# Optimization experiments

Measured on AMD Instinct MI355X. Metric: run time of the kernel, lower is better.

Reference implementation:

```python
import jax, jax.numpy as jnp
import numpy as np

NUM_GRAPHS = 16  # static number of graphs for pooling
BN_EPS = 1e-5


def gat_layer(x, W, a_src, a_dst, src, dst, N, concat):
    # x: (N, Fin), W: (H, Fin, Fout), a_src/a_dst: (H, Fout)
    Wh = jnp.einsum('ni,hio->hno', x, W)                      # (H, N, Fout)
    e_src = jnp.einsum('hno,ho->hn', Wh, a_src)               # (H, N)
    e_dst = jnp.einsum('hno,ho->hn', Wh, a_dst)               # (H, N)
    e = jax.nn.leaky_relu(e_src[:, src] + e_dst[:, dst], 0.2)  # (H, E)
    # edge softmax over incoming edges per dst; torch code starts max at 0
    seg_max = jax.vmap(lambda eh: jax.ops.segment_max(eh, dst, num_segments=N))(e)
    e_max = jnp.maximum(seg_max, 0.0)                         # (H, N)
    exp_e = jnp.exp(e - e_max[:, dst])                        # (H, E)
    exp_sum = jax.vmap(lambda eh: jax.ops.segment_sum(eh, dst, num_segments=N))(exp_e)
    attn = exp_e / (exp_sum[:, dst] + 1e-8)                   # (H, E)
    msgs = attn[:, :, None] * Wh[:, src]                      # (H, E, Fout)
    out = jax.vmap(lambda m: jax.ops.segment_sum(m, dst, num_segments=N))(msgs)  # (H, N, Fout)
    if concat:
        out = jnp.transpose(out, (1, 0, 2)).reshape(N, -1)
    else:
        out = out.mean(axis=0)
    return out, attn


def batchnorm(h, gamma, beta):
    mu = h.mean(axis=0)
    var = h.var(axis=0)
    return (h - mu) / jnp.sqrt(var + BN_EPS) * gamma + beta


def setup_inputs() -> dict:
    key = jax.random.key(0)
    ks = jax.random.split(key, 20)
    N, E = 50000, 400000
    IN, HID, H, NC = 262, 128, 4, 2

    def xavier(k, shape):
        fan_in, fan_out = shape[-2], shape[-1]
        lim = np.sqrt(6.0 / (fan_in + fan_out))
        return jax.random.uniform(k, shape, jnp.float32, -lim, lim)

    x = jax.random.normal(ks[0], (N, IN), jnp.float32)
    edge_index = jax.random.randint(ks[1], (2, E), 0, N, jnp.int64)
    batch = jnp.sort(jax.random.randint(ks[2], (N,), 0, NUM_GRAPHS, jnp.int64))

    return {
        'x': x, 'edge_index': edge_index, 'batch': batch,
        'W1': xavier(ks[3], (H, IN, HID)),
        'a_src1': xavier(ks[4], (H, HID, 1)).squeeze(-1),
        'a_dst1': xavier(ks[5], (H, HID, 1)).squeeze(-1),
        'W2': xavier(ks[6], (1, HID * H, HID)),
        'a_src2': xavier(ks[7], (1, HID, 1)).squeeze(-1),
        'a_dst2': xavier(ks[8], (1, HID, 1)).squeeze(-1),
        'bn1_g': jnp.ones((HID * H,), jnp.float32),
        'bn1_b': jnp.zeros((HID * H,), jnp.float32),
        'bn2_g': jnp.ones((HID,), jnp.float32),
        'bn2_b': jnp.zeros((HID,), jnp.float32),
        'cls_w1': xavier(ks[9], (HID, HID // 2)),
        'cls_b1': jnp.zeros((HID // 2,), jnp.float32),
        'cls_w2': xavier(ks[10], (HID // 2, NC)),
        'cls_b2': jnp.zeros((NC,), jnp.float32),
        'ep_w1': xavier(ks[11], (HID * 2, HID)),
        'ep_b1': jnp.zeros((HID,), jnp.float32),
        'ep_w2': xavier(ks[12], (HID, 1)),
        'ep_b2': jnp.zeros((1,), jnp.float32),
    }


def reference(x, edge_index, batch, W1, a_src1, a_dst1, W2, a_src2, a_dst2,
              bn1_g, bn1_b, bn2_g, bn2_b, cls_w1, cls_b1, cls_w2, cls_b2,
              ep_w1, ep_b1, ep_w2, ep_b2):
    N = x.shape[0]
    src, dst = edge_index[0], edge_index[1]

    h1, _ = gat_layer(x, W1, a_src1, a_dst1, src, dst, N, concat=True)
    h1 = batchnorm(jax.nn.elu(h1), bn1_g, bn1_b)

    h2, attn2 = gat_layer(h1, W2, a_src2, a_dst2, src, dst, N, concat=False)
    h2 = batchnorm(jax.nn.elu(h2), bn2_g, bn2_b)

    # global mean pool over graphs
    sums = jax.ops.segment_sum(h2, batch, num_segments=NUM_GRAPHS)
    counts = jax.ops.segment_sum(jnp.ones((N,), h2.dtype), batch, num_segments=NUM_GRAPHS)
    graph_repr = sums / jnp.clip(counts, 1.0)[:, None]

    logits = jax.nn.relu(graph_repr @ cls_w1 + cls_b1) @ cls_w2 + cls_b2

    edge_feat = jnp.concatenate([h2[src], h2[dst]], axis=1)  # (E, 2*hidden)
    importance = jax.nn.sigmoid(
        (jax.nn.relu(edge_feat @ ep_w1 + ep_b1) @ ep_w2 + ep_b2).squeeze(-1))

    gat_attention = jnp.transpose(attn2, (1, 0))  # (E, 1)
    return logits, h2, importance, gat_attention
```

## Files before the change

### kernel.cpp

```cpp
#include <hip/hip_runtime.h>
#include <hip/hip_bf16.h>
#include <math.h>

typedef __hip_bfloat16 bf16;
typedef __bf16 bf16x8 __attribute__((ext_vector_type(8)));
typedef __bf16 bf16x2v __attribute__((ext_vector_type(2)));
typedef float f32x4 __attribute__((ext_vector_type(4)));

#define NN 50000
#define EE 400000
#define FIN 262
#define KP1 288
#define HID 128
#define NH 4
#define C1 512
#define NGR 16
#define SCAN_NB ((NN + 255) / 256)

__device__ __forceinline__ float b2f(bf16 x){ return __bfloat162float(x); }
__device__ __forceinline__ bf16 f2b(float x){ return __float2bfloat16(x); }
__device__ __forceinline__ float lrelu(float v){ return v >= 0.f ? v : 0.2f * v; }
__device__ __forceinline__ float eluf(float v){ return v > 0.f ? v : expm1f(v); }

__global__ void zero_words(unsigned int* __restrict__ p, int n) {
  int i = blockIdx.x * 256 + threadIdx.x;
  if (i < n) p[i] = 0u;
}

__global__ __launch_bounds__(256)
void gemm_mfma(const bf16* __restrict__ A, const bf16* __restrict__ Bt,
               bf16* __restrict__ C, int M, int K, int Ncols,
               const float* __restrict__ sc, const float* __restrict__ sh) {
  __shared__ __align__(16) __bf16 As[128 * 40];
  __shared__ __align__(16) __bf16 Bs[128 * 40];
  int bm = blockIdx.y * 128, bn = blockIdx.x * 128;
  int tid = threadIdx.x;
  int wave = tid >> 6, lane = tid & 63;
  int quad = lane >> 4, l16 = lane & 15;
  int wm = (wave >> 1) * 64, wn = (wave & 1) * 64;
  f32x4 acc[4][4];
  #pragma unroll
  for (int i = 0; i < 4; ++i)
    #pragma unroll
    for (int j = 0; j < 4; ++j)
      acc[i][j] = (f32x4){0.f, 0.f, 0.f, 0.f};

  for (int k0 = 0; k0 < K; k0 += 32) {
    #pragma unroll
    for (int l = 0; l < 2; ++l) {
      int e = l * 2048 + tid * 8;
      int row = e >> 5, col = e & 31;
      uint4 va = {0u, 0u, 0u, 0u};
      int gm = bm + row;
      if (gm < M) {
        va = *(const uint4*)(A + (size_t)gm * K + k0 + col);
        if (sc) {
          bf16x8 a8 = *(bf16x8*)&va;
          float4 c0 = *(const float4*)(sc + k0 + col);
          float4 c1 = *(const float4*)(sc + k0 + col + 4);
          float4 h0 = *(const float4*)(sh + k0 + col);
          float4 h1v = *(const float4*)(sh + k0 + col + 4);
          bf16x8 t8;
          t8[0] = (__bf16)((float)a8[0] * c0.x + h0.x);
          t8[1] = (__bf16)((float)a8[1] * c0.y + h0.y);
          t8[2] = (__bf16)((float)a8[2] * c0.z + h0.z);
          t8[3] = (__bf16)((float)a8[3] * c0.w + h0.w);
          t8[4] = (__bf16)((float)a8[4] * c1.x + h1v.x);
          t8[5] = (__bf16)((float)a8[5] * c1.y + h1v.y);
          t8[6] = (__bf16)((float)a8[6] * c1.z + h1v.z);
          t8[7] = (__bf16)((float)a8[7] * c1.w + h1v.w);
          va = *(uint4*)&t8;
        }
      }
      *(uint4*)(&As[row * 40 + col]) = va;
      uint4 vb = {0u, 0u, 0u, 0u};
      int gn = bn + row;
      if (gn < Ncols) vb = *(const uint4*)(Bt + (size_t)gn * K + k0 + col);
      *(uint4*)(&Bs[row * 40 + col]) = vb;
    }
    __syncthreads();
    bf16x8 af[4], bf_[4];
    #pragma unroll
    for (int i = 0; i < 4; ++i)
      af[i] = *(const bf16x8*)(&As[(wm + i * 16 + l16) * 40 + quad * 8]);
    #pragma unroll
    for (int j = 0; j < 4; ++j)
      bf_[j] = *(const bf16x8*)(&Bs[(wn + j * 16 + l16) * 40 + quad * 8]);
    #pragma unroll
    for (int i = 0; i < 4; ++i)
      #pragma unroll
      for (int j = 0; j < 4; ++j)
        acc[i][j] = __builtin_amdgcn_mfma_f32_16x16x32_bf16(af[i], bf_[j], acc[i][j], 0, 0, 0);
    __syncthreads();
  }
  #pragma unroll
  for (int i = 0; i < 4; ++i) {
    #pragma unroll
    for (int r = 0; r < 4; ++r) {
      int gm = bm + wm + i * 16 + quad * 4 + r;
      if (gm >= M) continue;
      #pragma unroll
      for (int j = 0; j < 4; ++j) {
        int gn = bn + wn + j * 16 + l16;
        C[(size_t)gm * Ncols + gn] = f2b(acc[i][j][r]);
      }
    }
  }
}

__global__ void conv_x(const float* __restrict__ x, bf16* __restrict__ xb) {
  int i = blockIdx.x * 256 + threadIdx.x;
  if (i >= NN * KP1) return;
  int row = i / KP1, col = i - row * KP1;
  xb[i] = (col < FIN) ? f2b(x[(size_t)row * FIN + col]) : f2b(0.f);
}
__global__ void prep_b1t(const float* __restrict__ W1, bf16* __restrict__ B1t) {
  int i = blockIdx.x * 256 + threadIdx.x;
  if (i >= C1 * KP1) return;
  int n = i / KP1, k = i - n * KP1;
  int h = n >> 7, o = n & 127;
  B1t[i] = (k < FIN) ? f2b(W1[((size_t)h * FIN + k) * HID + o]) : f2b(0.f);
}
__global__ void prep_b2t(const float* __restrict__ W2, bf16* __restrict__ B2t) {
  int i = blockIdx.x * 256 + threadIdx.x;
  if (i >= HID * C1) return;
  int n = i >> 9, k = i & 511;
  B2t[i] = f2b(W2[(size_t)k * HID + n]);
}
__global__ void prep_bpt(const float* __restrict__ epw1, bf16* __restrict__ BPt) {
  int i = blockIdx.x * 256 + threadIdx.x;
  if (i >= 256 * HID) return;
  int n = i >> 7, k = i & 127;
  float v = (n < 128) ? epw1[(size_t)k * HID + n] : epw1[(size_t)(128 + k) * HID + (n - 128)];
  BPt[i] = f2b(v);
}

__global__ void edot_all(const bf16* __restrict__ Wh1, const float* __restrict__ av,
                         const float* __restrict__ bv, float* __restrict__ es1,
                         float* __restrict__ ed1) {
  int wid = threadIdx.x >> 6, lane = threadIdx.x & 63;
  int n = blockIdx.x * 4 + wid;
  if (n >= NN) return;
  int h = lane >> 4, c16 = lane & 15;
  int fbase = h * HID + c16 * 8;
  bf16x8 r = *(const bf16x8*)(Wh1 + (size_t)n * C1 + fbase);
  float s1 = 0.f, s2 = 0.f;
  #pragma unroll
  for (int j = 0; j < 8; ++j) {
    float rv = (float)r[j];
    s1 += rv * av[fbase + j];
    s2 += rv * bv[fbase + j];
  }
  #pragma unroll
  for (int off = 8; off > 0; off >>= 1) {
    s1 += __shfl_xor(s1, off);
    s2 += __shfl_xor(s2, off);
  }
  if (c16 == 0) { es1[n * 4 + h] = s1; ed1[n * 4 + h] = s2; }
}

__global__ void edot1(const bf16* __restrict__ Wh, const float* __restrict__ av,
                      const float* __restrict__ bv, float* __restrict__ es,
                      float* __restrict__ ed) {
  int wid = threadIdx.x >> 6, lane = threadIdx.x & 63;
  int r = blockIdx.x * 4 + wid;
  if (r >= NN) return;
  const bf16* row = Wh + (size_t)r * HID;
  float w0 = b2f(row[lane]), w1 = b2f(row[lane + 64]);
  float s1 = w0 * av[lane] + w1 * av[lane + 64];
  float s2 = w0 * bv[lane] + w1 * bv[lane + 64];
  #pragma unroll
  for (int off = 32; off > 0; off >>= 1) {
    s1 += __shfl_xor(s1, off);
    s2 += __shfl_xor(s2, off);
  }
  if (lane == 0) { es[r] = s1; ed[r] = s2; }
}

__global__ void count_kernel(const int* __restrict__ dst, int* __restrict__ deg, int E) {
  int e = blockIdx.x * blockDim.x + threadIdx.x;
  if (e >= E) return;
  int d = dst[e];
  if ((unsigned)d < NN) atomicAdd(&deg[d], 1);
}

__global__ void scan_p1(const int* __restrict__ deg, int* __restrict__ bsum) {
  __shared__ int s[256];
  int t = threadIdx.x;
  int i = blockIdx.x * 256 + t;
  s[t] = (i < NN) ? deg[i] : 0;
  __syncthreads();
  #pragma unroll
  for (int off = 128; off > 0; off >>= 1) {
    if (t < off) s[t] += s[t + off];
    __syncthreads();
  }
  if (t == 0) bsum[blockIdx.x] = s[0];
}
__global__ void scan_p2(const int* __restrict__ bsum, int* __restrict__ boff,
                        int* __restrict__ total_out) {
  __shared__ int s[256];
  int t = threadIdx.x;
  s[t] = (t < SCAN_NB) ? bsum[t] : 0;
  __syncthreads();
  if (t == 0) {
    int r = 0;
    for (int i = 0; i < SCAN_NB; ++i) { int v = s[i]; s[i] = r; r += v; }
    total_out[0] = r;
  }
  __syncthreads();
  if (t < SCAN_NB) boff[t] = s[t];
}
__global__ void scan_p3(const int* __restrict__ deg, const int* __restrict__ boff,
                        int* __restrict__ rowptr, int* __restrict__ cursor) {
  __shared__ int s[256];
  int t = threadIdx.x;
  int i = blockIdx.x * 256 + t;
  int v = (i < NN) ? deg[i] : 0;
  s[t] = v;
  __syncthreads();
  #pragma unroll
  for (int off = 1; off < 256; off <<= 1) {
    int add = (t >= off) ? s[t - off] : 0;
    __syncthreads();
    s[t] += add;
    __syncthreads();
  }
  if (i < NN) {
    int pos = boff[blockIdx.x] + s[t] - v;
    rowptr[i] = pos;
    cursor[i] = pos;
  }
}

__global__ void scatter_kernel(const int* __restrict__ src, const int* __restrict__ dst,
                               int* __restrict__ cursor, int* __restrict__ csr_s,
                               int* __restrict__ csr_d, int* __restrict__ csr_e, int E) {
  int e = blockIdx.x * blockDim.x + threadIdx.x;
  if (e >= E) return;
  int d = dst[e];
  if ((unsigned)d >= NN) return;
  int s = src[e]; if ((unsigned)s >= NN) s = 0;
  int p = atomicAdd(&cursor[d], 1);
  if ((unsigned)p < (unsigned)E) { csr_s[p] = s; csr_d[p] = d; csr_e[p] = e; }
}

__global__ void logits1(const int* __restrict__ csr_s, const int* __restrict__ csr_d,
                        const float4* __restrict__ es1, const float4* __restrict__ ed1,
                        float4* __restrict__ v1, int* __restrict__ m1i) {
  int j = blockIdx.x * 256 + threadIdx.x;
  if (j >= EE) return;
  int s = csr_s[j]; if ((unsigned)s >= NN) s = 0;
  int d = csr_d[j]; if ((unsigned)d >= NN) d = 0;
  float4 a = es1[s], bb = ed1[d];
  float4 v;
  v.x = lrelu(a.x + bb.x);
  v.y = lrelu(a.y + bb.y);
  v.z = lrelu(a.z + bb.z);
  v.w = lrelu(a.w + bb.w);
  v1[j] = v;
  if (v.x > 0.f) atomicMax(&m1i[d * 4 + 0], __float_as_int(v.x));
  if (v.y > 0.f) atomicMax(&m1i[d * 4 + 1], __float_as_int(v.y));
  if (v.z > 0.f) atomicMax(&m1i[d * 4 + 2], __float_as_int(v.z));
  if (v.w > 0.f) atomicMax(&m1i[d * 4 + 3], __float_as_int(v.w));
}

__global__ void logits2(const int* __restrict__ csr_s, const int* __restrict__ csr_d,
                        const float* __restrict__ es2, const float* __restrict__ ed2,
                        float* __restrict__ v2, int* __restrict__ m2i) {
  int j = blockIdx.x * 256 + threadIdx.x;
  if (j >= EE) return;
  int s = csr_s[j]; if ((unsigned)s >= NN) s = 0;
  int d = csr_d[j]; if ((unsigned)d >= NN) d = 0;
  float v = lrelu(es2[s] + ed2[d]);
  v2[j] = v;
  if (v > 0.f) atomicMax(&m2i[d], __float_as_int(v));
}

__global__ __launch_bounds__(256, 6)
void agg1_all(const int* __restrict__ csr_s, const int* __restrict__ rowptr,
              const float* __restrict__ lg, const float* __restrict__ mx,
              const bf16* __restrict__ Wh1, bf16* __restrict__ h1) {
  int wid = threadIdx.x >> 6, lane = threadIdx.x & 63;
  int node = blockIdx.x * 4 + wid;
  if (node >= NN) return;
  int b = rowptr[node], e = rowptr[node + 1];
  if (b < 0) b = 0; if (e > EE) e = EE;
  int h = lane >> 4;
  float m = mx[node * 4 + h];
  float sum = 0.f;
  float acc[8] = {};
  const bf16* W = Wh1 + lane * 8;
  int j = b;
  for (; j + 8 <= e; j += 8) {
    int s_[8]; float w[8];
    #pragma unroll
    for (int i = 0; i < 8; ++i) { s_[i] = csr_s[j + i]; w[i] = lg[(j + i) * 4 + h]; }
    bf16x8 r[8];
    #pragma unroll
    for (int i = 0; i < 8; ++i)
      r[i] = *(const bf16x8*)(W + (size_t)s_[i] * C1);
    #pragma unroll
    for (int i = 0; i < 8; ++i) {
      float p = __expf(w[i] - m);
      sum += p;
      #pragma unroll
      for (int k = 0; k < 8; ++k) acc[k] += p * (float)r[i][k];
    }
  }
  if (j + 4 <= e) {
    int s_[4]; float w[4];
    #pragma unroll
    for (int i = 0; i < 4; ++i) { s_[i] = csr_s[j + i]; w[i] = lg[(j + i) * 4 + h]; }
    bf16x8 r[4];
    #pragma unroll
    for (int i = 0; i < 4; ++i)
      r[i] = *(const bf16x8*)(W + (size_t)s_[i] * C1);
    #pragma unroll
    for (int i = 0; i < 4; ++i) {
      float p = __expf(w[i] - m);
      sum += p;
      #pragma unroll
      for (int k = 0; k < 8; ++k) acc[k] += p * (float)r[i][k];
    }
    j += 4;
  }
  for (; j < e; ++j) {
    int s0 = csr_s[j];
    float p = __expf(lg[j * 4 + h] - m);
    bf16x8 r0 = *(const bf16x8*)(W + (size_t)s0 * C1);
    sum += p;
    #pragma unroll
    for (int k = 0; k < 8; ++k) acc[k] += p * (float)r0[k];
  }
  float scale = 1.f / (sum + 1e-8f);
  bf16x8 o;
  #pragma unroll
  for (int k = 0; k < 8; ++k) o[k] = (__bf16)eluf(acc[k] * scale);
  *(bf16x8*)(h1 + (size_t)node * C1 + lane * 8) = o;
}

__global__ __launch_bounds__(256, 8)
void agg2_all(const int* __restrict__ csr_s, const int* __restrict__ rowptr,
              const float* __restrict__ lg, const float* __restrict__ mx,
              const bf16* __restrict__ Wh2, bf16* __restrict__ h2p,
              float* __restrict__ invs2) {
  int tid = threadIdx.x;
  int l16 = tid & 15;
  int node = blockIdx.x * 16 + (tid >> 4);
  if (node >= NN) return;
  int b = rowptr[node], e = rowptr[node + 1];
  if (b < 0) b = 0; if (e > EE) e = EE;
  float m = mx[node];
  float sum = 0.f;
  float acc[8] = {};
  const bf16* W = Wh2 + l16 * 8;
  int j = b;
  for (; j + 4 <= e; j += 4) {
    int s_[4]; float w[4];
    #pragma unroll
    for (int i = 0; i < 4; ++i) { s_[i] = csr_s[j + i]; w[i] = lg[j + i]; }
    bf16x8 r[4];
    #pragma unroll
    for (int i = 0; i < 4; ++i)
      r[i] = *(const bf16x8*)(W + (size_t)s_[i] * HID);
    #pragma unroll
    for (int i = 0; i < 4; ++i) {
      float p = __expf(w[i] - m);
      sum += p;
      #pragma unroll
      for (int k = 0; k < 8; ++k) acc[k] += p * (float)r[i][k];
    }
  }
  for (; j < e; ++j) {
    int s0 = csr_s[j];
    float p = __expf(lg[j] - m);
    bf16x8 r0 = *(const bf16x8*)(W + (size_t)s0 * HID);
    sum += p;
    #pragma unroll
    for (int k = 0; k < 8; ++k) acc[k] += p * (float)r0[k];
  }
  float scale = 1.f / (sum + 1e-8f);
  bf16x8 o;
  #pragma unroll
  for (int k = 0; k < 8; ++k) o[k] = (__bf16)eluf(acc[k] * scale);
  *(bf16x8*)(h2p + (size_t)node * HID + l16 * 8) = o;
  if (l16 == 0) invs2[node] = scale;
}

__global__ void attn_csr(const int* __restrict__ csr_d, const int* __restrict__ csr_e,
                         const float* __restrict__ lg, const float* __restrict__ mx,
                         const float* __restrict__ invs2, float* __restrict__ out) {
  int j = blockIdx.x * 256 + threadIdx.x;
  if (j >= EE) return;
  int d = csr_d[j]; if ((unsigned)d >= NN) d = 0;
  int e = csr_e[j]; if ((unsigned)e >= EE) return;
  out[e] = __expf(lg[j] - mx[d]) * invs2[d];
}

__global__ void stats_ro(const bf16* __restrict__ X, float* __restrict__ cs,
                         float* __restrict__ cq, int Nrows, int C) {
  int c = threadIdx.x;
  int rpb = (Nrows + gridDim.x - 1) / gridDim.x;
  int r0 = blockIdx.x * rpb, r1 = min(r0 + rpb, Nrows);
  float s = 0.f, s2 = 0.f;
  for (int r = r0; r < r1; ++r) {
    float v = b2f(X[(size_t)r * C + c]);
    s += v; s2 += v * v;
  }
  atomicAdd(&cs[c], s);
  atomicAdd(&cq[c], s2);
}

__global__ void bn_coef(const float* __restrict__ cs, const float* __restrict__ cq,
                        const float* __restrict__ gamma, const float* __restrict__ beta,
                        float* __restrict__ sc, float* __restrict__ sh, int C, float invN) {
  int c = blockIdx.x * 256 + threadIdx.x;
  if (c >= C) return;
  float mu = cs[c] * invN;
  float var = cq[c] * invN - mu * mu;
  float g = rsqrtf(fmaxf(var, 0.f) + 1e-5f) * gamma[c];
  sc[c] = g;
  sh[c] = beta[c] - mu * g;
}

__global__ void bn_out(const bf16* __restrict__ in, float* __restrict__ out2,
                       const float* __restrict__ sc, const float* __restrict__ sh) {
  int i = blockIdx.x * 256 + threadIdx.x;
  if (i >= NN * HID / 8) return;
  int c8 = (i & 15) * 8;
  bf16x8 v = *(const bf16x8*)(in + (size_t)i * 8);
  float o[8];
  #pragma unroll
  for (int k = 0; k < 8; ++k) o[k] = (float)v[k] * sc[c8 + k] + sh[c8 + k];
  *(float4*)(out2 + (size_t)i * 8)     = make_float4(o[0], o[1], o[2], o[3]);
  *(float4*)(out2 + (size_t)i * 8 + 4) = make_float4(o[4], o[5], o[6], o[7]);
}

__global__ __launch_bounds__(256)
void pool_kernel(const bf16* __restrict__ h2, const int* __restrict__ batch,
                 float* __restrict__ pooled) {
  int t = threadIdx.x;
  int f = t & 127, half = t >> 7;
  int r0 = blockIdx.x * 32;
  int g_cur = -1;
  float acc = 0.f;
  #pragma unroll
  for (int i = 0; i < 16; ++i) {
    int r = r0 + half + 2 * i;
    if (r >= NN) break;
    int g = batch[r]; if ((unsigned)g >= NGR) g = 0;
    float v = b2f(h2[(size_t)r * HID + f]);
    if (g != g_cur) {
      if (g_cur >= 0) atomicAdd(&pooled[g_cur * HID + f], acc);
      g_cur = g; acc = 0.f;
    }
    acc += v;
  }
  if (g_cur >= 0) atomicAdd(&pooled[g_cur * HID + f], acc);
}

__global__ void cnt_kernel(const int* __restrict__ batch, float* __restrict__ cnt) {
  int g = threadIdx.x;
  if (g >= NGR) return;
  int a = 0, b = NN;
  while (a < b) { int m = (a + b) >> 1; if (batch[m] < g) a = m + 1; else b = m; }
  int lb = a;
  a = 0; b = NN;
  while (a < b) { int m = (a + b) >> 1; if (batch[m] <= g) a = m + 1; else b = m; }
  cnt[g] = (float)(a - lb);
}

__global__ void cls_kernel(const float* __restrict__ pooled, const float* __restrict__ cnt,
                           const float* __restrict__ sc2, const float* __restrict__ sh2,
                           const float* __restrict__ w1, const float* __restrict__ b1,
                           const float* __restrict__ w2, const float* __restrict__ b2,
                           float* __restrict__ out) {
  __shared__ float repr[NGR * HID];
  __shared__ float hid[NGR * 64];
  int t = threadIdx.x;
  for (int i = t; i < NGR * HID; i += 128) {
    int g = i >> 7, c = i & 127;
    float c_ = cnt[g];
    repr[i] = (c_ > 0.f) ? (pooled[i] / c_ * sc2[c] + sh2[c]) : 0.f;
  }
  __syncthreads();
  for (int i = t; i < NGR * 64; i += 128) {
    int g = i >> 6, j = i & 63;
    float s = b1[j];
    for (int c = 0; c < HID; ++c) s += repr[g * HID + c] * w1[c * 64 + j];
    hid[i] = fmaxf(s, 0.f);
  }
  __syncthreads();
  if (t < NGR * 2) {
    int g = t >> 1, k = t & 1;
    float s = b2[k];
    for (int j = 0; j < 64; ++j) s += hid[g * 64 + j] * w2[j * 2 + k];
    out[t] = s;
  }
}

__global__ __launch_bounds__(256)
void eimp_kernel(const int* __restrict__ csr_s, const int* __restrict__ csr_d,
                 const int* __restrict__ csr_e, const bf16* __restrict__ PQ,
                 const float* __restrict__ b1, const float* __restrict__ w2,
                 const float* __restrict__ b2, float* __restrict__ out) {
  int tid = threadIdx.x;
  int wave = tid >> 6, lane = tid & 63;
  int g = lane >> 4, l16 = lane & 15;
  int slot = blockIdx.x * 16 + wave * 4 + g;
  if (slot >= EE) return;
  int s = csr_s[slot]; if ((unsigned)s >= NN) s = 0;
  int d = csr_d[slot]; if ((unsigned)d >= NN) d = 0;
  int e = csr_e[slot]; if ((unsigned)e >= EE) return;
  bf16x8 p = *(const bf16x8*)(PQ + (size_t)s * 256 + l16 * 8);
  bf16x8 q = *(const bf16x8*)(PQ + (size_t)d * 256 + 128 + l16 * 8);
  float acc = 0.f;
  #pragma unroll
  for (int r = 0; r < 8; ++r) {
    int jj = l16 * 8 + r;
    float hh = (float)p[r] + (float)q[r] + b1[jj];
    hh = fmaxf(hh, 0.f);
    acc += hh * w2[jj];
  }
  #pragma unroll
  for (int off = 8; off > 0; off >>= 1) acc += __shfl_xor(acc, off);
  if (l16 == 0) {
    float z = acc + b2[0];
    out[e] = 1.f / (1.f + expf(-z));
  }
}

extern "C" void kernel_launch(void* const* d_in, const int* in_sizes, int n_in,
                              void* d_out, int out_size, void* d_ws, size_t ws_size,
                              hipStream_t stream) {
  const float* x      = (const float*)d_in[0];
  const int*   ei     = (const int*)d_in[1];
  const int*   batch  = (const int*)d_in[2];
  const float* W1     = (const float*)d_in[3];
  const float* a_src1 = (const float*)d_in[4];
  const float* a_dst1 = (const float*)d_in[5];
  const float* W2     = (const float*)d_in[6];
  const float* a_src2 = (const float*)d_in[7];
  const float* a_dst2 = (const float*)d_in[8];
  const float* bn1_g  = (const float*)d_in[9];
  const float* bn1_b  = (const float*)d_in[10];
  const float* bn2_g  = (const float*)d_in[11];
  const float* bn2_b  = (const float*)d_in[12];
  const float* cls_w1 = (const float*)d_in[13];
  const float* cls_b1 = (const float*)d_in[14];
  const float* cls_w2 = (const float*)d_in[15];
  const float* cls_b2 = (const float*)d_in[16];
  const float* ep_w1  = (const float*)d_in[17];
  const float* ep_b1  = (const float*)d_in[18];
  const float* ep_w2  = (const float*)d_in[19];
  const float* ep_b2  = (const float*)d_in[20];

  const int* srcp = ei;
  const int* dstp = ei + EE;

  char* base = (char*)d_ws;
  bf16* xb   = (bf16*)(base);
  bf16* h1   = (bf16*)(base);
  bf16* Wh1  = (bf16*)(base + 51200000);
  bf16* Wh2  = (bf16*)(base + 51200000);
  bf16* PQ   = (bf16*)(base + 51200000);
  bf16* h2p  = (bf16*)(base + 76800000);
  float* es1   = (float*)(base + 102400000);
  float* ed1   = (float*)(base + 103200000);
  float* v2csr = (float*)(base + 102400000);
  int*   m1i   = (int*)(base + 104000000);
  int*   m2i   = (int*)(base + 104800000);
  int*   deg   = (int*)(base + 105000000);
  float* stats = (float*)(base + 105200000);
  float* cs1 = stats,        *cq1 = stats + 512;
  float* cs2 = stats + 1024, *cq2 = stats + 1152;
  float* pooled = stats + 1280;
  float* cnt    = stats + 3328;
  float* sc1   = (float*)(base + 105213376);
  float* sh1   = (float*)(base + 105215424);
  float* sc2   = (float*)(base + 105217472);
  float* sh2   = (float*)(base + 105217984);
  float* es2   = (float*)(base + 105218496);
  float* ed2   = (float*)(base + 105418496);
  float* invs2 = (float*)(base + 105618496);
  int*   cursor= (int*)(base + 105818496);
  int*   rowptr= (int*)(base + 106018496);
  int*   bsum  = (int*)(base + 106218560);
  int*   boff  = bsum + 256;
  int*   csr_s = (int*)(base + 106220608);
  int*   csr_d = (int*)(base + 107820608);
  int*   csr_e = (int*)(base + 109420608);
  float* v1csr = (float*)(base + 111020608);
  bf16*  B1t   = (bf16*)(base + 117420608);
  bf16*  B2t   = (bf16*)(base + 117715520);
  bf16*  BPt   = (bf16*)(base + 117846592);

  float* out        = (float*)d_out;
  float* out_logits = out;
  float* out_h2     = out + 32;
  float* out_imp    = out + 32 + (size_t)NN * HID;
  float* out_attn   = out_imp + EE;

  zero_words<<<(303344 + 255) / 256, 256, 0, stream>>>((unsigned int*)m1i, 303344);

  conv_x<<<(NN * KP1 + 255) / 256, 256, 0, stream>>>(x, xb);
  prep_b1t<<<(C1 * KP1 + 255) / 256, 256, 0, stream>>>(W1, B1t);
  prep_b2t<<<(HID * C1 + 255) / 256, 256, 0, stream>>>(W2, B2t);
  prep_bpt<<<(256 * HID + 255) / 256, 256, 0, stream>>>(ep_w1, BPt);

  count_kernel<<<(EE + 255) / 256, 256, 0, stream>>>(dstp, deg, EE);
  scan_p1<<<SCAN_NB, 256, 0, stream>>>(deg, bsum);
  scan_p2<<<1, 256, 0, stream>>>(bsum, boff, rowptr + NN);
  scan_p3<<<SCAN_NB, 256, 0, stream>>>(deg, boff, rowptr, cursor);
  scatter_kernel<<<(EE + 255) / 256, 256, 0, stream>>>(srcp, dstp, cursor,
                                                       csr_s, csr_d, csr_e, EE);

  dim3 g1(C1 / 128, (NN + 127) / 128);
  gemm_mfma<<<g1, 256, 0, stream>>>(xb, B1t, Wh1, NN, KP1, C1, nullptr, nullptr);
  edot_all<<<(NN + 3) / 4, 256, 0, stream>>>(Wh1, a_src1, a_dst1, es1, ed1);
  logits1<<<(EE + 255) / 256, 256, 0, stream>>>(csr_s, csr_d, (const float4*)es1,
                                                (const float4*)ed1, (float4*)v1csr, m1i);
  agg1_all<<<(NN + 3) / 4, 256, 0, stream>>>(csr_s, rowptr, v1csr,
                                             (const float*)m1i, Wh1, h1);

  stats_ro<<<400, C1, 0, stream>>>(h1, cs1, cq1, NN, C1);
  bn_coef<<<2, 256, 0, stream>>>(cs1, cq1, bn1_g, bn1_b, sc1, sh1, C1, 1.f / NN);

  dim3 g2(1, (NN + 127) / 128);
  gemm_mfma<<<g2, 256, 0, stream>>>(h1, B2t, Wh2, NN, C1, HID, sc1, sh1);
  edot1<<<(NN + 3) / 4, 256, 0, stream>>>(Wh2, a_src2, a_dst2, es2, ed2);
  logits2<<<(EE + 255) / 256, 256, 0, stream>>>(csr_s, csr_d, es2, ed2, v2csr, m2i);
  agg2_all<<<(NN + 15) / 16, 256, 0, stream>>>(csr_s, rowptr, v2csr,
                                               (const float*)m2i, Wh2, h2p, invs2);
  attn_csr<<<(EE + 255) / 256, 256, 0, stream>>>(csr_d, csr_e, v2csr,
                                                 (const float*)m2i, invs2, out_attn);

  pool_kernel<<<(NN + 31) / 32, 256, 0, stream>>>(h2p, batch, pooled);
  cnt_kernel<<<1, 64, 0, stream>>>(batch, cnt);

  stats_ro<<<400, HID, 0, stream>>>(h2p, cs2, cq2, NN, HID);
  bn_coef<<<1, 256, 0, stream>>>(cs2, cq2, bn2_g, bn2_b, sc2, sh2, HID, 1.f / NN);
  bn_out<<<(NN * HID / 8 + 255) / 256, 256, 0, stream>>>(h2p, out_h2, sc2, sh2);

  cls_kernel<<<1, 128, 0, stream>>>(pooled, cnt, sc2, sh2,
                                    cls_w1, cls_b1, cls_w2, cls_b2, out_logits);

  dim3 gpq(2, (NN + 127) / 128);
  gemm_mfma<<<gpq, 256, 0, stream>>>(h2p, BPt, PQ, NN, HID, 256, sc2, sh2);
  eimp_kernel<<<(EE + 15) / 16, 256, 0, stream>>>(csr_s, csr_d, csr_e, PQ,
                                                  ep_b1, ep_w2, ep_b2, out_imp);
}
```

Before: 631.5 us.

## Double-buffer GEMM shared tiles with register prefetch of the next K slice

The MFMA GEMM now keeps two LDS buffers and loads the next K tile from global memory into registers before running the MFMAs on the current tile. It then writes that prefetched tile into the other buffer, so only one barrier per iteration is needed. This is meant to hide global load latency behind matrix compute. The cost is doubled LDS use (about 40KB per block), which may reduce occupancy, plus extra registers for the prefetched data.

```diff
diff --git a/kernel.cpp b/kernel.cpp
--- a/kernel.cpp
+++ b/kernel.cpp
@@ -31,13 +31,19 @@
 void gemm_mfma(const bf16* __restrict__ A, const bf16* __restrict__ Bt,
                bf16* __restrict__ C, int M, int K, int Ncols,
                const float* __restrict__ sc, const float* __restrict__ sh) {
-  __shared__ __align__(16) __bf16 As[128 * 40];
-  __shared__ __align__(16) __bf16 Bs[128 * 40];
+  __shared__ __align__(16) __bf16 As[2][128 * 40];
+  __shared__ __align__(16) __bf16 Bs[2][128 * 40];
   int bm = blockIdx.y * 128, bn = blockIdx.x * 128;
   int tid = threadIdx.x;
   int wave = tid >> 6, lane = tid & 63;
   int quad = lane >> 4, l16 = lane & 15;
   int wm = (wave >> 1) * 64, wn = (wave & 1) * 64;
+  int rowA = (tid * 8) >> 5;
+  int colT = (tid * 8) & 31;
+  int gm0 = bm + rowA, gm1 = bm + rowA + 64;
+  int gn0 = bn + rowA, gn1 = bn + rowA + 64;
+  const uint4 zz = {0u, 0u, 0u, 0u};
+
   f32x4 acc[4][4];
   #pragma unroll
   for (int i = 0; i < 4; ++i)
@@ -45,54 +51,66 @@
     for (int j = 0; j < 4; ++j)
       acc[i][j] = (f32x4){0.f, 0.f, 0.f, 0.f};
 
-  for (int k0 = 0; k0 < K; k0 += 32) {
-    #pragma unroll
-    for (int l = 0; l < 2; ++l) {
-      int e = l * 2048 + tid * 8;
-      int row = e >> 5, col = e & 31;
-      uint4 va = {0u, 0u, 0u, 0u};
-      int gm = bm + row;
-      if (gm < M) {
-        va = *(const uint4*)(A + (size_t)gm * K + k0 + col);
-        if (sc) {
-          bf16x8 a8 = *(bf16x8*)&va;
-          float4 c0 = *(const float4*)(sc + k0 + col);
-          float4 c1 = *(const float4*)(sc + k0 + col + 4);
-          float4 h0 = *(const float4*)(sh + k0 + col);
-          float4 h1v = *(const float4*)(sh + k0 + col + 4);
-          bf16x8 t8;
-          t8[0] = (__bf16)((float)a8[0] * c0.x + h0.x);
-          t8[1] = (__bf16)((float)a8[1] * c0.y + h0.y);
-          t8[2] = (__bf16)((float)a8[2] * c0.z + h0.z);
-          t8[3] = (__bf16)((float)a8[3] * c0.w + h0.w);
-          t8[4] = (__bf16)((float)a8[4] * c1.x + h1v.x);
-          t8[5] = (__bf16)((float)a8[5] * c1.y + h1v.y);
-          t8[6] = (__bf16)((float)a8[6] * c1.z + h1v.z);
-          t8[7] = (__bf16)((float)a8[7] * c1.w + h1v.w);
-          va = *(uint4*)&t8;
-        }
-      }
-      *(uint4*)(&As[row * 40 + col]) = va;
-      uint4 vb = {0u, 0u, 0u, 0u};
-      int gn = bn + row;
-      if (gn < Ncols) vb = *(const uint4*)(Bt + (size_t)gn * K + k0 + col);
-      *(uint4*)(&Bs[row * 40 + col]) = vb;
-    }
-    __syncthreads();
-    bf16x8 af[4], bf_[4];
+  uint4 a0, a1, b0, b1;
+
+  auto xf = [&](uint4 v, int kb) -> uint4 {
+    if (sc == nullptr) return v;
+    bf16x8 a8 = *(bf16x8*)&v;
+    float4 c0 = *(const float4*)(sc + kb);
+    float4 c1 = *(const float4*)(sc + kb + 4);
+    float4 h0 = *(const float4*)(sh + kb);
+    float4 h1 = *(const float4*)(sh + kb + 4);
+    bf16x8 t8;
+    t8[0] = (__bf16)((float)a8[0] * c0.x + h0.x);
+    t8[1] = (__bf16)((float)a8[1] * c0.y + h0.y);
+    t8[2] = (__bf16)((float)a8[2] * c0.z + h0.z);
+    t8[3] = (__bf16)((float)a8[3] * c0.w + h0.w);
+    t8[4] = (__bf16)((float)a8[4] * c1.x + h1.x);
+    t8[5] = (__bf16)((float)a8[5] * c1.y + h1.y);
+    t8[6] = (__bf16)((float)a8[6] * c1.z + h1.z);
+    t8[7] = (__bf16)((float)a8[7] * c1.w + h1.w);
+    return *(uint4*)&t8;
+  };
+  auto ld = [&](int k0) {
+    a0 = (gm0 < M) ? *(const uint4*)(A + (size_t)gm0 * K + k0 + colT) : zz;
+    a1 = (gm1 < M) ? *(const uint4*)(A + (size_t)gm1 * K + k0 + colT) : zz;
+    b0 = (gn0 < Ncols) ? *(const uint4*)(Bt + (size_t)gn0 * K + k0 + colT) : zz;
+    b1 = (gn1 < Ncols) ? *(const uint4*)(Bt + (size_t)gn1 * K + k0 + colT) : zz;
+  };
+  auto st = [&](int buf, int k0) {
+    *(uint4*)(&As[buf][rowA * 40 + colT])        = xf(a0, k0 + colT);
+    *(uint4*)(&As[buf][(rowA + 64) * 40 + colT]) = xf(a1, k0 + colT);
+    *(uint4*)(&Bs[buf][rowA * 40 + colT])        = b0;
+    *(uint4*)(&Bs[buf][(rowA + 64) * 40 + colT]) = b1;
+  };
+
+  int nt = K >> 5;
+  ld(0);
+  st(0, 0);
+  __syncthreads();
+
+  for (int t = 0; t < nt; ++t) {
+    int cur = t & 1;
+    bool more = (t + 1 < nt);
+    if (more) ld((t + 1) << 5);
+
+    bf16x8 af[4], bfr[4];
     #pragma unroll
     for (int i = 0; i < 4; ++i)
-      af[i] = *(const bf16x8*)(&As[(wm + i * 16 + l16) * 40 + quad * 8]);
+      af[i] = *(const bf16x8*)(&As[cur][(wm + i * 16 + l16) * 40 + quad * 8]);
     #pragma unroll
     for (int j = 0; j < 4; ++j)
-      bf_[j] = *(const bf16x8*)(&Bs[(wn + j * 16 + l16) * 40 + quad * 8]);
+      bfr[j] = *(const bf16x8*)(&Bs[cur][(wn + j * 16 + l16) * 40 + quad * 8]);
     #pragma unroll
     for (int i = 0; i < 4; ++i)
       #pragma unroll
       for (int j = 0; j < 4; ++j)
-        acc[i][j] = __builtin_amdgcn_mfma_f32_16x16x32_bf16(af[i], bf_[j], acc[i][j], 0, 0, 0);
+        acc[i][j] = __builtin_amdgcn_mfma_f32_16x16x32_bf16(af[i], bfr[j], acc[i][j], 0, 0, 0);
+
+    if (more) st(cur ^ 1, (t + 1) << 5);
     __syncthreads();
   }
+
   #pragma unroll
   for (int i = 0; i < 4; ++i) {
     #pragma unroll
```

Measured after the change: 654.3 us. 3.6% more time.
